# Performance work log

Hardware: AMD Instinct MI355X
Metric: run time of the kernel (lower is better)

Reference implementation:

```python
import jax, jax.numpy as jnp
import numpy as np
from math import sqrt

THRESHOLD = 0.5
NEG_POS_RATIO = 3
ALPHA = 1.0


def make_priors():
    fms = [(38, 0.1, [1.0, 2.0, 0.5]), (19, 0.2, [1.0, 2.0, 0.5, 3.0, 1.0 / 3]),
           (10, 0.375, [1.0, 2.0, 0.5, 3.0, 1.0 / 3]), (5, 0.55, [1.0, 2.0, 0.5, 3.0, 1.0 / 3]),
           (3, 0.725, [1.0, 2.0, 0.5]), (1, 0.9, [1.0, 2.0, 0.5])]
    scales = [0.1, 0.2, 0.375, 0.55, 0.725, 0.9]
    priors = []
    for k, (d, s, ratios) in enumerate(fms):
        for i in range(d):
            for j in range(d):
                cx = (i + 0.5) / d
                cy = (j + 0.5) / d
                for r in ratios:
                    priors.append([cx, cy, s * sqrt(r), s / sqrt(r)])
                    if r == 1.0:
                        add = sqrt(scales[k] * scales[k + 1]) if k + 1 < len(scales) else 1.0
                        priors.append([cx, cy, add, add])
    return np.clip(np.asarray(priors, dtype=np.float32), 0.0, 1.0)  # [8732, 4]


def cxcy_to_xy(b):
    return jnp.concatenate([b[..., :2] - b[..., 2:] / 2.0, b[..., :2] + b[..., 2:] / 2.0], -1)


def jaccard(a, b):
    # a: [O,4] cxcy, b: [P,4] cxcy -> IoU [O,P]
    a_xy, b_xy = cxcy_to_xy(a), cxcy_to_xy(b)
    lt = jnp.maximum(a_xy[:, None, :2], b_xy[None, :, :2])
    rb = jnp.minimum(a_xy[:, None, 2:], b_xy[None, :, 2:])
    wh = jnp.clip(rb - lt, 0.0)
    inter = wh[..., 0] * wh[..., 1]
    area_a = (a_xy[:, 2] - a_xy[:, 0]) * (a_xy[:, 3] - a_xy[:, 1])
    area_b = (b_xy[:, 2] - b_xy[:, 0]) * (b_xy[:, 3] - b_xy[:, 1])
    return inter / (area_a[:, None] + area_b[None, :] - inter)


def cxcy_to_gcxgcy(cxcy, priors):
    g_cxcy = (cxcy[..., :2] - priors[..., :2]) / (priors[..., 2:] / 10.0)
    g_wh = jnp.log(cxcy[..., 2:] / priors[..., 2:]) * 5.0
    return jnp.concatenate([g_cxcy, g_wh], -1)


def match_one(boxes_i, priors):
    # boxes_i: [O,4] cxcy
    n_obj = boxes_i.shape[0]
    ov = jaccard(boxes_i, priors)                      # [O, P]
    ov_per_prior = ov.max(0)                           # [P]
    obj_per_prior = ov.argmax(0)                       # [P]
    prior_per_obj = ov.argmax(1)                       # [O]
    obj_per_prior = obj_per_prior.at[prior_per_obj].set(jnp.arange(n_obj))
    ov_per_prior = ov_per_prior.at[prior_per_obj].set(1.0)
    labels = (ov_per_prior >= THRESHOLD).astype(jnp.int32)  # [P], 1=text 0=bg
    true_locs = cxcy_to_gcxgcy(boxes_i[obj_per_prior], priors)  # [P,4]
    return labels, true_locs


def setup_inputs() -> dict:
    key = jax.random.key(0)
    k1, k2, k3, k4 = jax.random.split(key, 4)
    priors = jnp.asarray(make_priors())
    B, P, O = 512, priors.shape[0], 16
    predicted_locs = jax.random.normal(k1, (B, P, 4), dtype=jnp.float32)
    predicted_scores = jax.random.normal(k2, (B, P, 2), dtype=jnp.float32)
    centers = 0.2 + 0.6 * jax.random.uniform(k3, (B, O, 2), dtype=jnp.float32)
    wh = 0.05 + 0.35 * jax.random.uniform(k4, (B, O, 2), dtype=jnp.float32)
    boxes = jnp.concatenate([centers, wh], -1)  # cxcy format
    return {"predicted_locs": predicted_locs, "predicted_scores": predicted_scores,
            "boxes": boxes, "priors": priors}


def reference(predicted_locs, predicted_scores, boxes, priors):
    B, P, _ = predicted_locs.shape
    labels, true_locs = jax.vmap(match_one, in_axes=(0, None))(boxes, priors)  # [B,P], [B,P,4]
    pos = labels != 0
    mask = pos.astype(predicted_locs.dtype)            # [B,P]
    n_pos = pos.sum(1)                                 # [B]

    # localization L1 loss (mean over positive box coordinates)
    loc_abs = jnp.abs(predicted_locs - true_locs).sum(-1)  # [B,P]
    loc_loss = (loc_abs * mask).sum() / (mask.sum() * 4.0)

    # per-prior cross-entropy
    logp = jax.nn.log_softmax(predicted_scores, -1)
    ce = -jnp.take_along_axis(logp, labels[..., None], -1)[..., 0]  # [B,P]

    conf_pos = (ce * mask).sum()
    ce_neg = jnp.where(pos, 0.0, ce)
    ce_neg = jnp.sort(ce_neg, axis=1)[:, ::-1]         # descending
    hard = jnp.arange(P)[None, :] < (NEG_POS_RATIO * n_pos)[:, None]
    conf_hn = (ce_neg * hard.astype(ce_neg.dtype)).sum()
    conf_loss = (conf_pos + conf_hn) / n_pos.sum().astype(predicted_locs.dtype)
    return conf_loss + ALPHA * loc_loss
```

## Files before the change

kernel.cpp:

```cpp
#include <hip/hip_runtime.h>

#define NP 8732
#define NQ (NP / 4)
#define NO 16
#define BLK 256
#define NWAVE (BLK / 64)
#define SPLIT 4
#define CHUNK (NP / SPLIT)


__global__ __launch_bounds__(BLK, 2) void match_kernel(
    const float* __restrict__ boxes,
    const float* __restrict__ priors,
    unsigned char* __restrict__ g_obj,
    float* __restrict__ g_bv,
    int*   __restrict__ g_bi)
{
    const int b    = blockIdx.x;
    const int s    = blockIdx.y;
    const int tid  = threadIdx.x;
    const int lane = tid & 63;
    const int wv   = tid >> 6;
    const int par  = tid & 1;
    const int objLo = par << 3;
    const int lo = s * CHUNK, hi = lo + CHUNK;

    __shared__ float s_bxy[NO][4];
    __shared__ float s_barea[NO];
    __shared__ float s_redv[NO * NWAVE];
    __shared__ int   s_redi[NO * NWAVE];

    if (tid < NO) {
        const float* bx = boxes + (size_t)b * NO * 4 + tid * 4;
        float cx = bx[0], cy = bx[1], w = bx[2], h = bx[3];
        s_bxy[tid][0] = cx - w * 0.5f; s_bxy[tid][1] = cy - h * 0.5f;
        s_bxy[tid][2] = cx + w * 0.5f; s_bxy[tid][3] = cy + h * 0.5f;
        s_barea[tid] = w * h;
    }
    __syncthreads();

    float rx0[8], ry0[8], rx1[8], ry1[8], ra[8];
#pragma unroll
    for (int j = 0; j < 8; j++) {
        rx0[j] = s_bxy[objLo + j][0]; ry0[j] = s_bxy[objLo + j][1];
        rx1[j] = s_bxy[objLo + j][2]; ry1[j] = s_bxy[objLo + j][3];
        ra[j]  = s_barea[objLo + j];
    }

    float tbv[8]; int tbp[8];
#pragma unroll
    for (int j = 0; j < 8; j++) { tbv[j] = -1.0f; tbp[j] = lo; }

    unsigned char* obj_row = g_obj + (size_t)b * NP;
    for (int p = lo + (tid >> 1); p < hi; p += (BLK / 2)) {
        float4 pr = ((const float4*)priors)[p];
        float px0 = pr.x - pr.z * 0.5f, py0 = pr.y - pr.w * 0.5f;
        float px1 = pr.x + pr.z * 0.5f, py1 = pr.y + pr.w * 0.5f;
        float areab = pr.z * pr.w;
        float bv = -1.0f; int bo = objLo;
#pragma unroll
        for (int j = 0; j < 8; j++) {
            float ix0 = fmaxf(rx0[j], px0);
            float iy0 = fmaxf(ry0[j], py0);
            float ix1 = fminf(rx1[j], px1);
            float iy1 = fminf(ry1[j], py1);
            float iw = fmaxf(ix1 - ix0, 0.0f);
            float ih = fmaxf(iy1 - iy0, 0.0f);
            float inter = iw * ih;
            float den = ra[j] + areab - inter;
            float iou = inter * __builtin_amdgcn_rcpf(den);
            if (iou > bv)     { bv = iou; bo = objLo + j; }
            if (iou > tbv[j]) { tbv[j] = iou; tbp[j] = p; }
        }
        float vN = __shfl_xor(bv, 1, 64);
        int   oN = __shfl_xor(bo, 1, 64);
        bool take = par ? (vN >= bv) : (vN > bv);
        if (take) { bv = vN; bo = oN; }
        if (par == 0) {
            bool pos = (bv >= 0.5f);
            obj_row[p] = (unsigned char)(bo | (pos ? 0x80 : 0));
        }
    }

#pragma unroll
    for (int j = 0; j < 8; j++) {
        float v = tbv[j]; int i = tbp[j];
        for (int off = 32; off >= 2; off >>= 1) {
            float v2 = __shfl_down(v, off, 64);
            int   i2 = __shfl_down(i, off, 64);
            if (v2 > v || (v2 == v && i2 < i)) { v = v2; i = i2; }
        }
        if (lane < 2) {
            s_redv[(objLo + j) * NWAVE + wv] = v;
            s_redi[(objLo + j) * NWAVE + wv] = i;
        }
    }
    __syncthreads();
    if (tid < NO) {
        float v = s_redv[tid * NWAVE]; int i = s_redi[tid * NWAVE];
#pragma unroll
        for (int w = 1; w < NWAVE; w++) {
            float v2 = s_redv[tid * NWAVE + w]; int i2 = s_redi[tid * NWAVE + w];
            if (v2 > v || (v2 == v && i2 < i)) { v = v2; i = i2; }
        }
        g_bv[((size_t)b * NO + tid) * SPLIT + s] = v;
        g_bi[((size_t)b * NO + tid) * SPLIT + s] = i;
    }
}

__device__ __forceinline__ int hist_select(unsigned* hist, unsigned* s_part,
                                           unsigned* s_csuf, unsigned* s_sel,
                                           unsigned& kk, int tid, int lane, int wv)
{
    unsigned ps = 0;
#pragma unroll
    for (int i = 0; i < 16; i++) ps += hist[tid * 16 + i];
    s_part[tid] = ps;
    __syncthreads();
    if (wv == 0) {
        unsigned c0 = s_part[4 * lane + 0], c1 = s_part[4 * lane + 1];
        unsigned c2 = s_part[4 * lane + 2], c3 = s_part[4 * lane + 3];
        unsigned g = c0 + c1 + c2 + c3;
        unsigned incl = g;
#pragma unroll
        for (int off = 1; off < 64; off <<= 1) {
            unsigned o = __shfl_down(incl, off, 64);
            if (lane + off < 64) incl += o;
        }
        unsigned excl = incl - g;
        s_csuf[4 * lane + 3] = excl;
        s_csuf[4 * lane + 2] = excl + c3;
        s_csuf[4 * lane + 1] = excl + c3 + c2;
        s_csuf[4 * lane + 0] = excl + c3 + c2 + c1;
    }
    __syncthreads();
    unsigned base = s_csuf[tid];
    if (base < kk && kk <= base + s_part[tid]) {
        unsigned run = base;
        for (int i = 15; i >= 0; i--) {
            unsigned h = hist[tid * 16 + i];
            if (kk <= run + h) { s_sel[0] = (unsigned)(tid * 16 + i); s_sel[1] = kk - run; break; }
            run += h;
        }
    }
    __syncthreads();
    kk = s_sel[1];
    return (int)s_sel[0];
}

__global__ __launch_bounds__(BLK, 2) void loss_kernel(
    const float* __restrict__ plocs,
    const float* __restrict__ pscores,
    const float* __restrict__ boxes,
    const float* __restrict__ priors,
    const unsigned char* __restrict__ g_obj,
    const float* __restrict__ g_bv,
    const int*   __restrict__ g_bi,
    float* __restrict__ loc_out,
    float* __restrict__ conf_out,
    int*   __restrict__ npos_out)
{
    const int b    = blockIdx.x;
    const int tid  = threadIdx.x;
    const int lane = tid & 63;
    const int wv   = tid >> 6;

    __shared__ __align__(16) float s_ce[NP];
    __shared__ unsigned char s_obj[NP];
    __shared__ unsigned s_hist[4096];
    __shared__ unsigned s_part[256];
    __shared__ unsigned s_csuf[256];
    __shared__ unsigned s_sel[2];
    __shared__ float s_bcw[NO][4];
    __shared__ int   s_bestp[NO];
    __shared__ float s_fred[3 * NWAVE];
    __shared__ int   s_ired[NWAVE];

    const unsigned char* obj_row = g_obj + (size_t)b * NP;
    for (int p = tid; p < NP; p += BLK) s_obj[p] = obj_row[p];
    if (tid < NO * 4) ((float*)s_bcw)[tid] = boxes[(size_t)b * NO * 4 + tid];
    if (tid < NO) {
        const float* bv = g_bv + ((size_t)b * NO + tid) * SPLIT;
        const int*   bi = g_bi + ((size_t)b * NO + tid) * SPLIT;
        float v = bv[0]; int i = bi[0];
#pragma unroll
        for (int s = 1; s < SPLIT; s++) {
            float v2 = bv[s]; int i2 = bi[s];
            if (v2 > v || (v2 == v && i2 < i)) { v = v2; i = i2; }
        }
        s_bestp[tid] = i;
    }
    __syncthreads();
    if (tid == 0) {
#pragma unroll
        for (int o = 0; o < NO; o++) s_obj[s_bestp[o]] = (unsigned char)(0x80 | o);
    }
    __syncthreads();

    float loc_sum = 0.0f, conf_pos = 0.0f; int np = 0;
    const float2* sc2 = (const float2*)(pscores + (size_t)b * NP * 2);
    const float4* pl4 = (const float4*)(plocs  + (size_t)b * NP * 4);
    for (int p = tid; p < NP; p += BLK) {
        unsigned m = s_obj[p];
        bool pos = (m & 0x80) != 0;
        float2 s = sc2[p];
        float mx = fmaxf(s.x, s.y);
        float dd = fabsf(s.x - s.y);
        float lse = mx + __logf(1.0f + __expf(-dd));
        float ce = lse - (pos ? s.y : s.x);
        if (pos) {
            np++;
            conf_pos += ce;
            int o = m & 15;
            float4 pr = ((const float4*)priors)[p];
            float gx = (s_bcw[o][0] - pr.x) / (pr.z / 10.0f);
            float gy = (s_bcw[o][1] - pr.y) / (pr.w / 10.0f);
            float gw = __logf(s_bcw[o][2] / pr.z) * 5.0f;
            float gh = __logf(s_bcw[o][3] / pr.w) * 5.0f;
            float4 pl = pl4[p];
            loc_sum += fabsf(pl.x - gx) + fabsf(pl.y - gy)
                     + fabsf(pl.z - gw) + fabsf(pl.w - gh);
            s_ce[p] = 0.0f;
        } else {
            s_ce[p] = ce;
        }
    }

    int npw = np;
    for (int off = 32; off; off >>= 1) npw += __shfl_down(npw, off, 64);
    if (lane == 0) s_ired[wv] = npw;
    __syncthreads();
    int n_pos = 0;
#pragma unroll
    for (int w = 0; w < NWAVE; w++) n_pos += s_ired[w];

    const int K = 3 * n_pos;
    const bool selAll = (K >= NP);
    float t = 0.0f;
    const float4* ce4 = (const float4*)s_ce;
    if (!selAll) {
        unsigned kk = (unsigned)K;
        for (int i = tid; i < 4096; i += BLK) s_hist[i] = 0u;
        __syncthreads();
        for (int q = tid; q < NQ; q += BLK) {
            float4 v = ce4[q];
            atomicAdd(&s_hist[__float_as_uint(v.x) >> 19], 1u);
            atomicAdd(&s_hist[__float_as_uint(v.y) >> 19], 1u);
            atomicAdd(&s_hist[__float_as_uint(v.z) >> 19], 1u);
            atomicAdd(&s_hist[__float_as_uint(v.w) >> 19], 1u);
        }
        __syncthreads();
        unsigned b1 = (unsigned)hist_select(s_hist, s_part, s_csuf, s_sel, kk, tid, lane, wv);
        for (int i = tid; i < 4096; i += BLK) s_hist[i] = 0u;
        __syncthreads();
        for (int q = tid; q < NQ; q += BLK) {
            float4 v = ce4[q];
#pragma unroll
            for (int j = 0; j < 4; j++) {
                unsigned u = __float_as_uint(j == 0 ? v.x : j == 1 ? v.y : j == 2 ? v.z : v.w);
                if ((u >> 19) == b1) atomicAdd(&s_hist[(u >> 7) & 0xFFFu], 1u);
            }
        }
        __syncthreads();
        unsigned b2 = (unsigned)hist_select(s_hist, s_part, s_csuf, s_sel, kk, tid, lane, wv);
        unsigned p2 = (b1 << 12) | b2;
        for (int i = tid; i < 4096; i += BLK) s_hist[i] = 0u;
        __syncthreads();
        for (int q = tid; q < NQ; q += BLK) {
            float4 v = ce4[q];
#pragma unroll
            for (int j = 0; j < 4; j++) {
                unsigned u = __float_as_uint(j == 0 ? v.x : j == 1 ? v.y : j == 2 ? v.z : v.w);
                if ((u >> 7) == p2) atomicAdd(&s_hist[u & 0x7Fu], 1u);
            }
        }
        __syncthreads();
        unsigned b3 = (unsigned)hist_select(s_hist, s_part, s_csuf, s_sel, kk, tid, lane, wv);
        t = __uint_as_float((p2 << 7) | b3);
    }

    float sgt = 0.0f; int cgt = 0;
    for (int q = tid; q < NQ; q += BLK) {
        float4 v = ce4[q];
        if (selAll || v.x > t) { sgt += v.x; cgt++; }
        if (selAll || v.y > t) { sgt += v.y; cgt++; }
        if (selAll || v.z > t) { sgt += v.z; cgt++; }
        if (selAll || v.w > t) { sgt += v.w; cgt++; }
    }

    float a = sgt, c = conf_pos, l = loc_sum; int g = cgt;
    for (int off = 32; off; off >>= 1) {
        a += __shfl_down(a, off, 64);
        c += __shfl_down(c, off, 64);
        l += __shfl_down(l, off, 64);
        g += __shfl_down(g, off, 64);
    }
    __syncthreads();
    if (lane == 0) {
        s_fred[wv] = a; s_fred[NWAVE + wv] = c; s_fred[2 * NWAVE + wv] = l;
        s_ired[wv] = g;
    }
    __syncthreads();
    if (tid == 0) {
        float sa = 0.0f, sc = 0.0f, sl = 0.0f; int sg = 0;
#pragma unroll
        for (int w = 0; w < NWAVE; w++) {
            sa += s_fred[w]; sc += s_fred[NWAVE + w]; sl += s_fred[2 * NWAVE + w];
            sg += s_ired[w];
        }
        float conf_hn = selAll ? sa : (sa + (float)(K - sg) * t);
        conf_out[b] = sc + conf_hn;
        loc_out[b]  = sl;
        npos_out[b] = n_pos;
    }
}

__global__ __launch_bounds__(BLK, 2) void mbox_row_kernel(
    const float* __restrict__ plocs, const float* __restrict__ pscores,
    const float* __restrict__ boxes, const float* __restrict__ priors,
    float* __restrict__ loc_out, float* __restrict__ conf_out,
    int* __restrict__ npos_out)
{
    const int b = blockIdx.x, tid = threadIdx.x, lane = tid & 63, wv = tid >> 6;
    const int par = tid & 1, objLo = par << 3;
    __shared__ __align__(16) float s_ce[NP];
    __shared__ unsigned char s_obj[NP];
    __shared__ float s_bcw[NO][4], s_bxy[NO][4], s_barea[NO];
    __shared__ float s_redv[NO * NWAVE]; __shared__ int s_redi[NO * NWAVE];
    __shared__ int s_bestp[NO];
    __shared__ unsigned s_hist16[16];
    __shared__ float s_tval;
    __shared__ float s_fred[3 * NWAVE]; __shared__ int s_ired[NWAVE];

    if (tid < NO * 4) ((float*)s_bcw)[tid] = boxes[(size_t)b * NO * 4 + tid];
    __syncthreads();
    if (tid < NO) {
        float cx = s_bcw[tid][0], cy = s_bcw[tid][1], w = s_bcw[tid][2], h = s_bcw[tid][3];
        s_bxy[tid][0] = cx - w * 0.5f; s_bxy[tid][1] = cy - h * 0.5f;
        s_bxy[tid][2] = cx + w * 0.5f; s_bxy[tid][3] = cy + h * 0.5f;
        s_barea[tid] = w * h;
    }
    __syncthreads();
    float rx0[8], ry0[8], rx1[8], ry1[8], ra[8];
#pragma unroll
    for (int j = 0; j < 8; j++) {
        rx0[j] = s_bxy[objLo + j][0]; ry0[j] = s_bxy[objLo + j][1];
        rx1[j] = s_bxy[objLo + j][2]; ry1[j] = s_bxy[objLo + j][3];
        ra[j]  = s_barea[objLo + j];
    }
    float tbv[8]; int tbp[8];
#pragma unroll
    for (int j = 0; j < 8; j++) { tbv[j] = -1.0f; tbp[j] = 0; }
    for (int p = (tid >> 1); p < NP; p += (BLK / 2)) {
        float4 pr = ((const float4*)priors)[p];
        float px0 = pr.x - pr.z * 0.5f, py0 = pr.y - pr.w * 0.5f;
        float px1 = pr.x + pr.z * 0.5f, py1 = pr.y + pr.w * 0.5f;
        float areab = pr.z * pr.w;
        float bv = -1.0f; int bo = objLo;
#pragma unroll
        for (int j = 0; j < 8; j++) {
            float ix0 = fmaxf(rx0[j], px0), iy0 = fmaxf(ry0[j], py0);
            float ix1 = fminf(rx1[j], px1), iy1 = fminf(ry1[j], py1);
            float iw = fmaxf(ix1 - ix0, 0.0f), ih = fmaxf(iy1 - iy0, 0.0f);
            float inter = iw * ih, den = ra[j] + areab - inter;
            float iou = inter * __builtin_amdgcn_rcpf(den);
            if (iou > bv) { bv = iou; bo = objLo + j; }
            if (iou > tbv[j]) { tbv[j] = iou; tbp[j] = p; }
        }
        float vN = __shfl_xor(bv, 1, 64); int oN = __shfl_xor(bo, 1, 64);
        bool take = par ? (vN >= bv) : (vN > bv);
        if (take) { bv = vN; bo = oN; }
        if (par == 0) s_obj[p] = (unsigned char)(bo | ((bv >= 0.5f) ? 0x80 : 0));
    }
#pragma unroll
    for (int j = 0; j < 8; j++) {
        float v = tbv[j]; int i = tbp[j];
        for (int off = 32; off >= 2; off >>= 1) {
            float v2 = __shfl_down(v, off, 64); int i2 = __shfl_down(i, off, 64);
            if (v2 > v || (v2 == v && i2 < i)) { v = v2; i = i2; }
        }
        if (lane < 2) { s_redv[(objLo + j) * NWAVE + wv] = v; s_redi[(objLo + j) * NWAVE + wv] = i; }
    }
    __syncthreads();
    if (tid < NO) {
        float v = s_redv[tid * NWAVE]; int i = s_redi[tid * NWAVE];
#pragma unroll
        for (int w = 1; w < NWAVE; w++) {
            float v2 = s_redv[tid * NWAVE + w]; int i2 = s_redi[tid * NWAVE + w];
            if (v2 > v || (v2 == v && i2 < i)) { v = v2; i = i2; }
        }
        s_bestp[tid] = i;
    }
    __syncthreads();
    if (tid == 0) {
#pragma unroll
        for (int o = 0; o < NO; o++) s_obj[s_bestp[o]] = (unsigned char)(0x80 | o);
    }
    __syncthreads();
    float loc_sum = 0.0f, conf_pos = 0.0f; int np = 0;
    const float2* sc2 = (const float2*)(pscores + (size_t)b * NP * 2);
    const float4* pl4 = (const float4*)(plocs + (size_t)b * NP * 4);
    for (int p = tid; p < NP; p += BLK) {
        unsigned m = s_obj[p]; bool pos = (m & 0x80) != 0;
        float2 s = sc2[p];
        float mx = fmaxf(s.x, s.y), dd = fabsf(s.x - s.y);
        float ce = mx + __logf(1.0f + __expf(-dd)) - (pos ? s.y : s.x);
        if (pos) {
            np++; conf_pos += ce;
            int o = m & 15;
            float4 pr = ((const float4*)priors)[p];
            float gx = (s_bcw[o][0] - pr.x) / (pr.z / 10.0f);
            float gy = (s_bcw[o][1] - pr.y) / (pr.w / 10.0f);
            float gw = __logf(s_bcw[o][2] / pr.z) * 5.0f;
            float gh = __logf(s_bcw[o][3] / pr.w) * 5.0f;
            float4 pl = pl4[p];
            loc_sum += fabsf(pl.x - gx) + fabsf(pl.y - gy) + fabsf(pl.z - gw) + fabsf(pl.w - gh);
            s_ce[p] = 0.0f;
        } else s_ce[p] = ce;
    }
    int npw = np;
    for (int off = 32; off; off >>= 1) npw += __shfl_down(npw, off, 64);
    if (lane == 0) s_ired[wv] = npw;
    __syncthreads();
    int n_pos = 0;
#pragma unroll
    for (int w = 0; w < NWAVE; w++) n_pos += s_ired[w];
    const int K = 3 * n_pos; const bool selAll = (K >= NP);
    float t = 0.0f;
    const float4* ce4 = (const float4*)s_ce;
    if (!selAll) {
        unsigned prefix = 0u, kk = (unsigned)K; bool done = false;
        for (int shift = 28; shift >= 0 && !done; shift -= 4) {
            __syncthreads();
            if (tid < 16) s_hist16[tid] = 0u;
            __syncthreads();
            unsigned maskhi = (shift == 28) ? 0u : (0xFFFFFFFFu << (shift + 4));
            for (int q = tid; q < NQ; q += BLK) {
                float4 v = ce4[q];
#pragma unroll
                for (int j = 0; j < 4; j++) {
                    unsigned u = __float_as_uint(j == 0 ? v.x : j == 1 ? v.y : j == 2 ? v.z : v.w);
                    if ((u & maskhi) == prefix) atomicAdd(&s_hist16[(u >> shift) & 15u], 1u);
                }
            }
            __syncthreads();
            int dsel = 15; unsigned cnt;
            for (;; dsel--) { cnt = s_hist16[dsel]; if (kk <= cnt || dsel == 0) break; kk -= cnt; }
            prefix |= ((unsigned)dsel << shift);
            if (shift > 0 && cnt == 1u) {
                unsigned mh = 0xFFFFFFFFu << shift;
                for (int q = tid; q < NQ; q += BLK) {
                    float4 v = ce4[q];
#pragma unroll
                    for (int j = 0; j < 4; j++) {
                        float f = (j == 0 ? v.x : j == 1 ? v.y : j == 2 ? v.z : v.w);
                        if ((__float_as_uint(f) & mh) == prefix) s_tval = f;
                    }
                }
                __syncthreads();
                t = s_tval; done = true;
            } else if (shift == 0) t = __uint_as_float(prefix);
        }
    }
    float sgt = 0.0f; int cgt = 0;
    for (int q = tid; q < NQ; q += BLK) {
        float4 v = ce4[q];
        if (selAll || v.x > t) { sgt += v.x; cgt++; }
        if (selAll || v.y > t) { sgt += v.y; cgt++; }
        if (selAll || v.z > t) { sgt += v.z; cgt++; }
        if (selAll || v.w > t) { sgt += v.w; cgt++; }
    }
    float a = sgt, c = conf_pos, l = loc_sum; int g = cgt;
    for (int off = 32; off; off >>= 1) {
        a += __shfl_down(a, off, 64); c += __shfl_down(c, off, 64);
        l += __shfl_down(l, off, 64); g += __shfl_down(g, off, 64);
    }
    __syncthreads();
    if (lane == 0) { s_fred[wv] = a; s_fred[NWAVE + wv] = c; s_fred[2 * NWAVE + wv] = l; s_ired[wv] = g; }
    __syncthreads();
    if (tid == 0) {
        float sa = 0, sc = 0, sl = 0; int sg = 0;
#pragma unroll
        for (int w = 0; w < NWAVE; w++) { sa += s_fred[w]; sc += s_fred[NWAVE + w]; sl += s_fred[2 * NWAVE + w]; sg += s_ired[w]; }
        float conf_hn = selAll ? sa : (sa + (float)(K - sg) * t);
        conf_out[b] = sc + conf_hn; loc_out[b] = sl; npos_out[b] = n_pos;
    }
}

__global__ __launch_bounds__(256) void mbox_finalize_kernel(
    const float* __restrict__ loc_in, const float* __restrict__ conf_in,
    const int* __restrict__ npos_in, int B, float* __restrict__ out)
{
    __shared__ float sl[4], sc[4];
    __shared__ int si[4];
    int tid = threadIdx.x, lane = tid & 63, wv = tid >> 6;
    float l = 0.0f, c = 0.0f; int n = 0;
    for (int i = tid; i < B; i += 256) { l += loc_in[i]; c += conf_in[i]; n += npos_in[i]; }
    for (int off = 32; off; off >>= 1) {
        l += __shfl_down(l, off, 64);
        c += __shfl_down(c, off, 64);
        n += __shfl_down(n, off, 64);
    }
    if (lane == 0) { sl[wv] = l; sc[wv] = c; si[wv] = n; }
    __syncthreads();
    if (tid == 0) {
        float tl = sl[0] + sl[1] + sl[2] + sl[3];
        float tc = sc[0] + sc[1] + sc[2] + sc[3];
        int tn = si[0] + si[1] + si[2] + si[3];
        float fn = (float)tn;
        out[0] = tc / fn + tl / (fn * 4.0f);
    }
}

extern "C" void kernel_launch(void* const* d_in, const int* in_sizes, int n_in,
                              void* d_out, int out_size, void* d_ws, size_t ws_size,
                              hipStream_t stream) {
    const float* plocs   = (const float*)d_in[0];
    const float* pscores = (const float*)d_in[1];
    const float* boxes   = (const float*)d_in[2];
    const float* priors  = (const float*)d_in[3];
    const int B = in_sizes[0] / (NP * 4);

    float* loc_ws  = (float*)d_ws;
    float* conf_ws = loc_ws + B;
    int*   np_ws   = (int*)(conf_ws + B);
    float* g_bv    = (float*)(np_ws + B);
    int*   g_bi    = (int*)(g_bv + (size_t)B * NO * SPLIT);
    unsigned char* g_obj = (unsigned char*)(g_bi + (size_t)B * NO * SPLIT);
    size_t need = (size_t)(3 * B) * 4 + (size_t)B * NO * SPLIT * 8 + (size_t)B * NP;

    if (ws_size >= need) {
        match_kernel<<<dim3(B, SPLIT), BLK, 0, stream>>>(boxes, priors, g_obj, g_bv, g_bi);
        loss_kernel<<<B, BLK, 0, stream>>>(plocs, pscores, boxes, priors,
                                           g_obj, g_bv, g_bi, loc_ws, conf_ws, np_ws);
    } else {
        mbox_row_kernel<<<B, BLK, 0, stream>>>(plocs, pscores, boxes, priors,
                                               loc_ws, conf_ws, np_ws);
    }
    mbox_finalize_kernel<<<1, 256, 0, stream>>>(loc_ws, conf_ws, np_ws, B, (float*)d_out);
}
```

Baseline: 201.0 us.

## Keep CE values in registers, early-exit radix select, split matching across quads

The match kernel now gives each prior to four threads handling four objects each instead of two threads with eight, and raises the launch-bounds occupancy hint. Adjacent lanes merge with an extra xor-shuffle stage. In the loss kernel, per-prior cross-entropy values stay in a 35-entry register array rather than shared memory, so each histogram pass reads registers. The radix select exits early when the chosen bucket holds one element, and the object row is copied into shared memory with 32-bit words. This trades higher register pressure (possible spills) for fewer LDS round trips and fewer histogram passes.

```diff
diff --git a/kernel.cpp b/kernel.cpp
--- a/kernel.cpp
+++ b/kernel.cpp
@@ -2,6 +2,7 @@
 
 #define NP 8732
 #define NQ (NP / 4)
+#define NPT 35
 #define NO 16
 #define BLK 256
 #define NWAVE (BLK / 64)
@@ -9,7 +10,7 @@
 #define CHUNK (NP / SPLIT)
 
 
-__global__ __launch_bounds__(BLK, 2) void match_kernel(
+__global__ __launch_bounds__(BLK, 8) void match_kernel(
     const float* __restrict__ boxes,
     const float* __restrict__ priors,
     unsigned char* __restrict__ g_obj,
@@ -21,8 +22,8 @@
     const int tid  = threadIdx.x;
     const int lane = tid & 63;
     const int wv   = tid >> 6;
-    const int par  = tid & 1;
-    const int objLo = par << 3;
+    const int quad = tid & 3;
+    const int objLo = quad << 2;
     const int lo = s * CHUNK, hi = lo + CHUNK;
 
     __shared__ float s_bxy[NO][4];
@@ -39,27 +40,27 @@
     }
     __syncthreads();
 
-    float rx0[8], ry0[8], rx1[8], ry1[8], ra[8];
-#pragma unroll
-    for (int j = 0; j < 8; j++) {
+    float rx0[4], ry0[4], rx1[4], ry1[4], ra[4];
+#pragma unroll
+    for (int j = 0; j < 4; j++) {
         rx0[j] = s_bxy[objLo + j][0]; ry0[j] = s_bxy[objLo + j][1];
         rx1[j] = s_bxy[objLo + j][2]; ry1[j] = s_bxy[objLo + j][3];
         ra[j]  = s_barea[objLo + j];
     }
 
-    float tbv[8]; int tbp[8];
-#pragma unroll
-    for (int j = 0; j < 8; j++) { tbv[j] = -1.0f; tbp[j] = lo; }
+    float tbv[4]; int tbp[4];
+#pragma unroll
+    for (int j = 0; j < 4; j++) { tbv[j] = -1.0f; tbp[j] = lo; }
 
     unsigned char* obj_row = g_obj + (size_t)b * NP;
-    for (int p = lo + (tid >> 1); p < hi; p += (BLK / 2)) {
+    for (int p = lo + (tid >> 2); p < hi; p += (BLK / 4)) {
         float4 pr = ((const float4*)priors)[p];
         float px0 = pr.x - pr.z * 0.5f, py0 = pr.y - pr.w * 0.5f;
         float px1 = pr.x + pr.z * 0.5f, py1 = pr.y + pr.w * 0.5f;
         float areab = pr.z * pr.w;
         float bv = -1.0f; int bo = objLo;
 #pragma unroll
-        for (int j = 0; j < 8; j++) {
+        for (int j = 0; j < 4; j++) {
             float ix0 = fmaxf(rx0[j], px0);
             float iy0 = fmaxf(ry0[j], py0);
             float ix1 = fminf(rx1[j], px1);
@@ -74,23 +75,27 @@
         }
         float vN = __shfl_xor(bv, 1, 64);
         int   oN = __shfl_xor(bo, 1, 64);
-        bool take = par ? (vN >= bv) : (vN > bv);
+        bool take = (quad & 1) ? (vN >= bv) : (vN > bv);
         if (take) { bv = vN; bo = oN; }
-        if (par == 0) {
+        vN = __shfl_xor(bv, 2, 64);
+        oN = __shfl_xor(bo, 2, 64);
+        take = (quad & 2) ? (vN >= bv) : (vN > bv);
+        if (take) { bv = vN; bo = oN; }
+        if (quad == 0) {
             bool pos = (bv >= 0.5f);
             obj_row[p] = (unsigned char)(bo | (pos ? 0x80 : 0));
         }
     }
 
 #pragma unroll
-    for (int j = 0; j < 8; j++) {
+    for (int j = 0; j < 4; j++) {
         float v = tbv[j]; int i = tbp[j];
-        for (int off = 32; off >= 2; off >>= 1) {
+        for (int off = 32; off >= 4; off >>= 1) {
             float v2 = __shfl_down(v, off, 64);
             int   i2 = __shfl_down(i, off, 64);
             if (v2 > v || (v2 == v && i2 < i)) { v = v2; i = i2; }
         }
-        if (lane < 2) {
+        if (lane < 4) {
             s_redv[(objLo + j) * NWAVE + wv] = v;
             s_redi[(objLo + j) * NWAVE + wv] = i;
         }
@@ -165,7 +170,6 @@
     const int lane = tid & 63;
     const int wv   = tid >> 6;
 
-    __shared__ __align__(16) float s_ce[NP];
     __shared__ unsigned char s_obj[NP];
     __shared__ unsigned s_hist[4096];
     __shared__ unsigned s_part[256];
@@ -173,11 +177,12 @@
     __shared__ unsigned s_sel[2];
     __shared__ float s_bcw[NO][4];
     __shared__ int   s_bestp[NO];
+    __shared__ float s_tval;
     __shared__ float s_fred[3 * NWAVE];
     __shared__ int   s_ired[NWAVE];
 
-    const unsigned char* obj_row = g_obj + (size_t)b * NP;
-    for (int p = tid; p < NP; p += BLK) s_obj[p] = obj_row[p];
+    const unsigned* objw = (const unsigned*)(g_obj + (size_t)b * NP);
+    for (int i = tid; i < NP / 4; i += BLK) ((unsigned*)s_obj)[i] = objw[i];
     if (tid < NO * 4) ((float*)s_bcw)[tid] = boxes[(size_t)b * NO * 4 + tid];
     if (tid < NO) {
         const float* bv = g_bv + ((size_t)b * NO + tid) * SPLIT;
@@ -197,33 +202,38 @@
     }
     __syncthreads();
 
+    float ce[NPT];
     float loc_sum = 0.0f, conf_pos = 0.0f; int np = 0;
     const float2* sc2 = (const float2*)(pscores + (size_t)b * NP * 2);
     const float4* pl4 = (const float4*)(plocs  + (size_t)b * NP * 4);
-    for (int p = tid; p < NP; p += BLK) {
-        unsigned m = s_obj[p];
-        bool pos = (m & 0x80) != 0;
-        float2 s = sc2[p];
-        float mx = fmaxf(s.x, s.y);
-        float dd = fabsf(s.x - s.y);
-        float lse = mx + __logf(1.0f + __expf(-dd));
-        float ce = lse - (pos ? s.y : s.x);
-        if (pos) {
-            np++;
-            conf_pos += ce;
-            int o = m & 15;
-            float4 pr = ((const float4*)priors)[p];
-            float gx = (s_bcw[o][0] - pr.x) / (pr.z / 10.0f);
-            float gy = (s_bcw[o][1] - pr.y) / (pr.w / 10.0f);
-            float gw = __logf(s_bcw[o][2] / pr.z) * 5.0f;
-            float gh = __logf(s_bcw[o][3] / pr.w) * 5.0f;
-            float4 pl = pl4[p];
-            loc_sum += fabsf(pl.x - gx) + fabsf(pl.y - gy)
-                     + fabsf(pl.z - gw) + fabsf(pl.w - gh);
-            s_ce[p] = 0.0f;
-        } else {
-            s_ce[p] = ce;
-        }
+#pragma unroll
+    for (int k = 0; k < NPT; k++) {
+        int p = tid + k * BLK;
+        float v = 0.0f;
+        if (p < NP) {
+            unsigned m = s_obj[p];
+            bool pos = (m & 0x80) != 0;
+            float2 s = sc2[p];
+            float mx = fmaxf(s.x, s.y);
+            float dd = fabsf(s.x - s.y);
+            float cev = mx + __logf(1.0f + __expf(-dd)) - (pos ? s.y : s.x);
+            if (pos) {
+                np++;
+                conf_pos += cev;
+                int o = m & 15;
+                float4 pr = ((const float4*)priors)[p];
+                float gx = (s_bcw[o][0] - pr.x) / (pr.z / 10.0f);
+                float gy = (s_bcw[o][1] - pr.y) / (pr.w / 10.0f);
+                float gw = __logf(s_bcw[o][2] / pr.z) * 5.0f;
+                float gh = __logf(s_bcw[o][3] / pr.w) * 5.0f;
+                float4 pl = pl4[p];
+                loc_sum += fabsf(pl.x - gx) + fabsf(pl.y - gy)
+                         + fabsf(pl.z - gw) + fabsf(pl.w - gh);
+            } else {
+                v = cev;
+            }
+        }
+        ce[k] = v;
     }
 
     int npw = np;
@@ -237,55 +247,62 @@
     const int K = 3 * n_pos;
     const bool selAll = (K >= NP);
     float t = 0.0f;
-    const float4* ce4 = (const float4*)s_ce;
     if (!selAll) {
         unsigned kk = (unsigned)K;
         for (int i = tid; i < 4096; i += BLK) s_hist[i] = 0u;
         __syncthreads();
-        for (int q = tid; q < NQ; q += BLK) {
-            float4 v = ce4[q];
-            atomicAdd(&s_hist[__float_as_uint(v.x) >> 19], 1u);
-            atomicAdd(&s_hist[__float_as_uint(v.y) >> 19], 1u);
-            atomicAdd(&s_hist[__float_as_uint(v.z) >> 19], 1u);
-            atomicAdd(&s_hist[__float_as_uint(v.w) >> 19], 1u);
-        }
+#pragma unroll
+        for (int k = 0; k < NPT; k++)
+            atomicAdd(&s_hist[__float_as_uint(ce[k]) >> 19], 1u);
         __syncthreads();
         unsigned b1 = (unsigned)hist_select(s_hist, s_part, s_csuf, s_sel, kk, tid, lane, wv);
-        for (int i = tid; i < 4096; i += BLK) s_hist[i] = 0u;
-        __syncthreads();
-        for (int q = tid; q < NQ; q += BLK) {
-            float4 v = ce4[q];
-#pragma unroll
-            for (int j = 0; j < 4; j++) {
-                unsigned u = __float_as_uint(j == 0 ? v.x : j == 1 ? v.y : j == 2 ? v.z : v.w);
+        unsigned cnt1 = s_hist[b1];
+        if (cnt1 == 1u) {
+#pragma unroll
+            for (int k = 0; k < NPT; k++)
+                if ((__float_as_uint(ce[k]) >> 19) == b1) s_tval = ce[k];
+            __syncthreads();
+            t = s_tval;
+        } else {
+            __syncthreads();
+            for (int i = tid; i < 4096; i += BLK) s_hist[i] = 0u;
+            __syncthreads();
+#pragma unroll
+            for (int k = 0; k < NPT; k++) {
+                unsigned u = __float_as_uint(ce[k]);
                 if ((u >> 19) == b1) atomicAdd(&s_hist[(u >> 7) & 0xFFFu], 1u);
             }
-        }
-        __syncthreads();
-        unsigned b2 = (unsigned)hist_select(s_hist, s_part, s_csuf, s_sel, kk, tid, lane, wv);
-        unsigned p2 = (b1 << 12) | b2;
-        for (int i = tid; i < 4096; i += BLK) s_hist[i] = 0u;
-        __syncthreads();
-        for (int q = tid; q < NQ; q += BLK) {
-            float4 v = ce4[q];
-#pragma unroll
-            for (int j = 0; j < 4; j++) {
-                unsigned u = __float_as_uint(j == 0 ? v.x : j == 1 ? v.y : j == 2 ? v.z : v.w);
-                if ((u >> 7) == p2) atomicAdd(&s_hist[u & 0x7Fu], 1u);
+            __syncthreads();
+            unsigned b2 = (unsigned)hist_select(s_hist, s_part, s_csuf, s_sel, kk, tid, lane, wv);
+            unsigned p2 = (b1 << 12) | b2;
+            unsigned cnt2 = s_hist[b2];
+            if (cnt2 == 1u) {
+#pragma unroll
+                for (int k = 0; k < NPT; k++)
+                    if ((__float_as_uint(ce[k]) >> 7) == p2) s_tval = ce[k];
+                __syncthreads();
+                t = s_tval;
+            } else {
+                __syncthreads();
+                for (int i = tid; i < 4096; i += BLK) s_hist[i] = 0u;
+                __syncthreads();
+#pragma unroll
+                for (int k = 0; k < NPT; k++) {
+                    unsigned u = __float_as_uint(ce[k]);
+                    if ((u >> 7) == p2) atomicAdd(&s_hist[u & 0x7Fu], 1u);
+                }
+                __syncthreads();
+                unsigned b3 = (unsigned)hist_select(s_hist, s_part, s_csuf, s_sel, kk, tid, lane, wv);
+                t = __uint_as_float((p2 << 7) | b3);
             }
         }
-        __syncthreads();
-        unsigned b3 = (unsigned)hist_select(s_hist, s_part, s_csuf, s_sel, kk, tid, lane, wv);
-        t = __uint_as_float((p2 << 7) | b3);
     }
 
     float sgt = 0.0f; int cgt = 0;
-    for (int q = tid; q < NQ; q += BLK) {
-        float4 v = ce4[q];
-        if (selAll || v.x > t) { sgt += v.x; cgt++; }
-        if (selAll || v.y > t) { sgt += v.y; cgt++; }
-        if (selAll || v.z > t) { sgt += v.z; cgt++; }
-        if (selAll || v.w > t) { sgt += v.w; cgt++; }
+#pragma unroll
+    for (int k = 0; k < NPT; k++) {
+        float v = ce[k];
+        if (selAll || v > t) { sgt += v; cgt++; }
     }
 
     float a = sgt, c = conf_pos, l = loc_sum; int g = cgt;
@@ -404,9 +421,9 @@
         unsigned m = s_obj[p]; bool pos = (m & 0x80) != 0;
         float2 s = sc2[p];
         float mx = fmaxf(s.x, s.y), dd = fabsf(s.x - s.y);
-        float ce = mx + __logf(1.0f + __expf(-dd)) - (pos ? s.y : s.x);
+        float cev = mx + __logf(1.0f + __expf(-dd)) - (pos ? s.y : s.x);
         if (pos) {
-            np++; conf_pos += ce;
+            np++; conf_pos += cev;
             int o = m & 15;
             float4 pr = ((const float4*)priors)[p];
             float gx = (s_bcw[o][0] - pr.x) / (pr.z / 10.0f);
@@ -416,7 +433,7 @@
             float4 pl = pl4[p];
             loc_sum += fabsf(pl.x - gx) + fabsf(pl.y - gy) + fabsf(pl.z - gw) + fabsf(pl.w - gh);
             s_ce[p] = 0.0f;
-        } else s_ce[p] = ce;
+        } else s_ce[p] = cev;
     }
     int npw = np;
     for (int off = 32; off; off >>= 1) npw += __shfl_down(npw, off, 64);
```

Result: faster. 196.6 us (-2.2%).
